# Optimization experiments

Measured on AMD Instinct MI355X. Metric: run time of the kernel, lower is better.

Reference implementation:

```python
import jax, jax.numpy as jnp
import numpy as np

L = 65536   # path length
D = 6       # path channels
K = 4       # signature truncation depth (max of sig_orders)


def setup_inputs() -> dict:
    key = jax.random.key(0)
    # scale keeps high-order signature terms numerically tame over 65k steps
    x = jax.random.normal(key, (L, D), dtype=jnp.float32) * 0.05
    return {"x": x}


def _signature(x):
    """Truncated path signature (levels 1..K), flattened, via Chen's relation.

    Signature of one linear segment with increment dx is exp(dx) in the
    tensor algebra: level k term = dx^{(x)k} / k!.  Full-path signature is the
    Chen (tensor-algebra) product of the per-segment exponentials, computed
    with a left-fold scan over increments.
    """
    dx = x[1:] - x[:-1]                       # (N, D) increments
    N = dx.shape[0]
    # Vectorized exp(dx) levels: E[k-1] = dx^{(x)k}/k!, flattened (N, D^k)
    E = [dx]
    for k in range(2, K + 1):
        Ek = jnp.einsum('na,nb->nab', E[-1], dx).reshape(N, -1) / k
        E.append(Ek)

    S0 = tuple(jnp.zeros((D ** (k + 1),), dtype=x.dtype) for k in range(K))

    def chen(S, e):
        # T_k = S_k + e_k + sum_{i=1}^{k-1} S_i (x) e_{k-i}   (S_0 = e_0 = 1)
        T = []
        for k in range(K):
            t = S[k] + e[k]
            for i in range(k):
                t = t + jnp.einsum('a,b->ab', S[i], e[k - 1 - i]).reshape(-1)
            T.append(t)
        return tuple(T), None

    S, _ = jax.lax.scan(chen, S0, tuple(E))
    # flatten levels 1..K: shape (D + D^2 + ... + D^K,) = (1554,)
    return jnp.concatenate(S)


def reference(x):
    return _signature(x)
```

## Files before the change

### kernel.cpp

```cpp
#include <hip/hip_runtime.h>

#define DIM 6
#define NSEG 65535
#define CH 32
#define NCHUNK 2048

#define PSTRIDE 1568
#define PL1 0
#define PL2 8
#define PL3 48
#define PL4 264

__global__ __launch_bounds__(64) void sig_fold(const float* __restrict__ x,
                                               float* __restrict__ part) {
    __shared__ float dxs[CH * 8];
    const int t = threadIdx.x;
    const int c = blockIdx.x;
    const int j0 = c * CH;
    const int cnt = min(CH, NSEG - j0);

    for (int f = t; f < CH * 8; f += 64) dxs[f] = 0.f;
    __syncthreads();
    const float* xb = x + (size_t)j0 * DIM;
    for (int f = t; f < cnt * DIM; f += 64) {
        int j = f / 6, k = f - j * 6;
        dxs[j * 8 + k] = xb[f + 6] - xb[f];
    }
    __syncthreads();

    const int ab = (t < 36) ? t : 35;
    const int a = ab / 6, b = ab - a * 6;
    const float* dxap = dxs + a;
    const float* dxbp = dxs + b;

    float r4[36], r3[6], r2 = 0.f, s1 = 0.f;
#pragma unroll
    for (int i = 0; i < 36; ++i) r4[i] = 0.f;
#pragma unroll
    for (int i = 0; i < 6; ++i) r3[i] = 0.f;

#pragma unroll 2
    for (int j = 0; j < CH; ++j) {
        const float4 q0 = *(const float4*)(dxs + j * 8);
        const float2 q1 = *(const float2*)(dxs + j * 8 + 4);
        const float dxv[6] = {q0.x, q0.y, q0.z, q0.w, q1.x, q1.y};
        const float dxa = dxap[j * 8];
        const float dxb = dxbp[j * 8];

        float t2 = fmaf(dxb, fmaf(dxa, (1.f / 12.f), s1 * (1.f / 3.f)), r2);
        float t2h = 0.5f * t2;
        float w[6];
#pragma unroll
        for (int cc = 0; cc < 6; ++cc) w[cc] = fmaf(t2h, dxv[cc], r3[cc]);
#pragma unroll
        for (int cc = 0; cc < 6; ++cc)
#pragma unroll
            for (int d = 0; d < 6; ++d)
                r4[cc * 6 + d] = fmaf(w[cc], dxv[d], r4[cc * 6 + d]);
        float t3 = fmaf(dxa, (1.f / 3.f), s1);
        float v = fmaf(0.5f * t3, dxb, r2);
#pragma unroll
        for (int cc = 0; cc < 6; ++cc) r3[cc] = fmaf(v, dxv[cc], r3[cc]);
        r2 = fmaf(fmaf(0.5f, dxa, s1), dxb, r2);
        s1 += dxa;
    }

    if (t < 36) {
        float* P = part + (size_t)c * PSTRIDE;
        if (a == b) P[PL1 + a] = s1;
        P[PL2 + ab] = r2;
        float* p3 = P + PL3 + ab * 6;
        *(float2*)(p3 + 0) = make_float2(r3[0], r3[1]);
        *(float2*)(p3 + 2) = make_float2(r3[2], r3[3]);
        *(float2*)(p3 + 4) = make_float2(r3[4], r3[5]);
        float* p4 = P + PL4 + ab * 36;
#pragma unroll
        for (int i = 0; i < 9; ++i)
            *(float4*)(p4 + 4 * i) =
                make_float4(r4[4 * i], r4[4 * i + 1], r4[4 * i + 2], r4[4 * i + 3]);
    }
}

__global__ __launch_bounds__(64) void sig_comb(const float* __restrict__ in,
                                               float* __restrict__ out,
                                               int R, int flat_out) {
    const int t = threadIdx.x;
    const int ab = (t < 36) ? t : 35;
    const int a = ab / 6, b = ab - a * 6;
    const float* base = in + (size_t)blockIdx.x * R * PSTRIDE;

    float r4[36], r3[6], r2, s1;
    {
        const float* P = base;
        s1 = P[PL1 + a];
        r2 = P[PL2 + ab];
        const float* p3 = P + PL3 + ab * 6;
#pragma unroll
        for (int i = 0; i < 3; ++i) {
            float2 q = *(const float2*)(p3 + 2 * i);
            r3[2 * i] = q.x; r3[2 * i + 1] = q.y;
        }
        const float* p4 = P + PL4 + ab * 36;
#pragma unroll
        for (int i = 0; i < 9; ++i) {
            float4 q = *(const float4*)(p4 + 4 * i);
            r4[4 * i] = q.x; r4[4 * i + 1] = q.y;
            r4[4 * i + 2] = q.z; r4[4 * i + 3] = q.w;
        }
    }

    for (int r = 1; r < R; ++r) {
        const float* U = base + (size_t)r * PSTRIDE;
        float b1[6];
#pragma unroll
        for (int d = 0; d < 6; ++d) b1[d] = U[PL1 + d];
        float b2[36];
#pragma unroll
        for (int i = 0; i < 9; ++i) {
            float4 q = *(const float4*)(U + PL2 + 4 * i);
            b2[4 * i] = q.x; b2[4 * i + 1] = q.y;
            b2[4 * i + 2] = q.z; b2[4 * i + 3] = q.w;
        }
        float b1a = U[PL1 + a];
        float b1b = U[PL1 + b];
        float b2ab = U[PL2 + ab];
        float b2rb[6];
        {
            const float* p = U + PL2 + b * 6;
#pragma unroll
            for (int i = 0; i < 3; ++i) {
                float2 q = *(const float2*)(p + 2 * i);
                b2rb[2 * i] = q.x; b2rb[2 * i + 1] = q.y;
            }
        }
        float b3ab[6];
        {
            const float* p = U + PL3 + ab * 6;
#pragma unroll
            for (int i = 0; i < 3; ++i) {
                float2 q = *(const float2*)(p + 2 * i);
                b3ab[2 * i] = q.x; b3ab[2 * i + 1] = q.y;
            }
        }
        float b3b[36];
        {
            const float* p = U + PL3 + b * 36;
#pragma unroll
            for (int i = 0; i < 9; ++i) {
                float4 q = *(const float4*)(p + 4 * i);
                b3b[4 * i] = q.x; b3b[4 * i + 1] = q.y;
                b3b[4 * i + 2] = q.z; b3b[4 * i + 3] = q.w;
            }
        }
        float b4[36];
        {
            const float* p = U + PL4 + ab * 36;
#pragma unroll
            for (int i = 0; i < 9; ++i) {
                float4 q = *(const float4*)(p + 4 * i);
                b4[4 * i] = q.x; b4[4 * i + 1] = q.y;
                b4[4 * i + 2] = q.z; b4[4 * i + 3] = q.w;
            }
        }

#pragma unroll
        for (int cc = 0; cc < 6; ++cc)
#pragma unroll
            for (int d = 0; d < 6; ++d) {
                const int cd = cc * 6 + d;
                float v = r4[cd] + b4[cd];
                v = fmaf(r3[cc], b1[d], v);
                v = fmaf(r2, b2[cd], v);
                r4[cd] = fmaf(s1, b3b[cd], v);
            }
#pragma unroll
        for (int cc = 0; cc < 6; ++cc) {
            float v = r3[cc] + b3ab[cc];
            v = fmaf(r2, b1[cc], v);
            r3[cc] = fmaf(s1, b2rb[cc], v);
        }
        r2 = fmaf(s1, b1b, r2 + b2ab);
        s1 += b1a;
    }

    if (t < 36) {
        if (flat_out) {
            float* O = out;
            if (a == b) O[a] = s1;
            O[6 + ab] = r2;
            float* o3 = O + 42 + ab * 6;
#pragma unroll
            for (int i = 0; i < 3; ++i)
                *(float2*)(o3 + 2 * i) = make_float2(r3[2 * i], r3[2 * i + 1]);
            float* o4 = O + 258 + ab * 36;
#pragma unroll
            for (int i = 0; i < 18; ++i)
                *(float2*)(o4 + 2 * i) = make_float2(r4[2 * i], r4[2 * i + 1]);
        } else {
            float* P = out + (size_t)blockIdx.x * PSTRIDE;
            if (a == b) P[PL1 + a] = s1;
            P[PL2 + ab] = r2;
            float* p3 = P + PL3 + ab * 6;
#pragma unroll
            for (int i = 0; i < 3; ++i)
                *(float2*)(p3 + 2 * i) = make_float2(r3[2 * i], r3[2 * i + 1]);
            float* p4 = P + PL4 + ab * 36;
#pragma unroll
            for (int i = 0; i < 9; ++i)
                *(float4*)(p4 + 4 * i) =
                    make_float4(r4[4 * i], r4[4 * i + 1], r4[4 * i + 2], r4[4 * i + 3]);
        }
    }
}

extern "C" void kernel_launch(void* const* d_in, const int* in_sizes, int n_in,
                              void* d_out, int out_size, void* d_ws, size_t ws_size,
                              hipStream_t stream) {
    const float* x = (const float*)d_in[0];
    float* out = (float*)d_out;
    float* ws0 = (float*)d_ws;
    float* ws1 = ws0 + (size_t)NCHUNK * PSTRIDE;
    float* ws2 = ws1 + (size_t)256 * PSTRIDE;

    sig_fold<<<NCHUNK, 64, 0, stream>>>(x, ws0);
    sig_comb<<<256, 64, 0, stream>>>(ws0, ws1, 8, 0);
    sig_comb<<<16, 64, 0, stream>>>(ws1, ws2, 16, 0);
    sig_comb<<<1, 64, 0, stream>>>(ws2, out, 16, 1);
}
```

Measured before the change: 114.3 us.

## Stage combine inputs in LDS, use 4-level 8-way tree, select dx via masks

The combine kernel now copies its R partial signatures into shared memory with coalesced float4 loads before the sequential Chen-product loop, so the many per-thread loads hit LDS instead of global memory. The reduction tree changes from 256→16→1 with fan-in 16 to 256→32→4→1 with fan-in 8, which fits the shared buffer and shortens each block's serial chain at the cost of one extra launch. In the fold kernel, per-thread dx[a] and dx[b] are picked from the broadcast row with mask FMAs instead of separate indexed LDS reads, and the loop is unrolled further. The risks are higher LDS use per block, an extra launch, and more VALU work in the fold loop.

```diff
diff --git a/kernel.cpp b/kernel.cpp
--- a/kernel.cpp
+++ b/kernel.cpp
@@ -30,8 +30,12 @@
 
     const int ab = (t < 36) ? t : 35;
     const int a = ab / 6, b = ab - a * 6;
-    const float* dxap = dxs + a;
-    const float* dxbp = dxs + b;
+    float ma[6], mb[6];
+#pragma unroll
+    for (int k = 0; k < 6; ++k) {
+        ma[k] = (a == k) ? 1.f : 0.f;
+        mb[k] = (b == k) ? 1.f : 0.f;
+    }
 
     float r4[36], r3[6], r2 = 0.f, s1 = 0.f;
 #pragma unroll
@@ -39,13 +43,17 @@
 #pragma unroll
     for (int i = 0; i < 6; ++i) r3[i] = 0.f;
 
-#pragma unroll 2
+#pragma unroll 4
     for (int j = 0; j < CH; ++j) {
         const float4 q0 = *(const float4*)(dxs + j * 8);
         const float2 q1 = *(const float2*)(dxs + j * 8 + 4);
         const float dxv[6] = {q0.x, q0.y, q0.z, q0.w, q1.x, q1.y};
-        const float dxa = dxap[j * 8];
-        const float dxb = dxbp[j * 8];
+        float dxa = 0.f, dxb = 0.f;
+#pragma unroll
+        for (int k = 0; k < 6; ++k) {
+            dxa = fmaf(ma[k], dxv[k], dxa);
+            dxb = fmaf(mb[k], dxv[k], dxb);
+        }
 
         float t2 = fmaf(dxb, fmaf(dxa, (1.f / 12.f), s1 * (1.f / 3.f)), r2);
         float t2h = 0.5f * t2;
@@ -84,14 +92,22 @@
 __global__ __launch_bounds__(64) void sig_comb(const float* __restrict__ in,
                                                float* __restrict__ out,
                                                int R, int flat_out) {
+    __shared__ float U[8 * PSTRIDE];
     const int t = threadIdx.x;
     const int ab = (t < 36) ? t : 35;
     const int a = ab / 6, b = ab - a * 6;
-    const float* base = in + (size_t)blockIdx.x * R * PSTRIDE;
+
+    {
+        const float4* g4 = (const float4*)(in + (size_t)blockIdx.x * R * PSTRIDE);
+        float4* s4 = (float4*)U;
+        const int nf4 = R * (PSTRIDE / 4);
+        for (int i = t; i < nf4; i += 64) s4[i] = g4[i];
+    }
+    __syncthreads();
 
     float r4[36], r3[6], r2, s1;
     {
-        const float* P = base;
+        const float* P = U;
         s1 = P[PL1 + a];
         r2 = P[PL2 + ab];
         const float* p3 = P + PL3 + ab * 6;
@@ -110,23 +126,23 @@
     }
 
     for (int r = 1; r < R; ++r) {
-        const float* U = base + (size_t)r * PSTRIDE;
+        const float* Us = U + r * PSTRIDE;
         float b1[6];
 #pragma unroll
-        for (int d = 0; d < 6; ++d) b1[d] = U[PL1 + d];
+        for (int d = 0; d < 6; ++d) b1[d] = Us[PL1 + d];
         float b2[36];
 #pragma unroll
         for (int i = 0; i < 9; ++i) {
-            float4 q = *(const float4*)(U + PL2 + 4 * i);
+            float4 q = *(const float4*)(Us + PL2 + 4 * i);
             b2[4 * i] = q.x; b2[4 * i + 1] = q.y;
             b2[4 * i + 2] = q.z; b2[4 * i + 3] = q.w;
         }
-        float b1a = U[PL1 + a];
-        float b1b = U[PL1 + b];
-        float b2ab = U[PL2 + ab];
+        float b1a = Us[PL1 + a];
+        float b1b = Us[PL1 + b];
+        float b2ab = Us[PL2 + ab];
         float b2rb[6];
         {
-            const float* p = U + PL2 + b * 6;
+            const float* p = Us + PL2 + b * 6;
 #pragma unroll
             for (int i = 0; i < 3; ++i) {
                 float2 q = *(const float2*)(p + 2 * i);
@@ -135,7 +151,7 @@
         }
         float b3ab[6];
         {
-            const float* p = U + PL3 + ab * 6;
+            const float* p = Us + PL3 + ab * 6;
 #pragma unroll
             for (int i = 0; i < 3; ++i) {
                 float2 q = *(const float2*)(p + 2 * i);
@@ -144,7 +160,7 @@
         }
         float b3b[36];
         {
-            const float* p = U + PL3 + b * 36;
+            const float* p = Us + PL3 + b * 36;
 #pragma unroll
             for (int i = 0; i < 9; ++i) {
                 float4 q = *(const float4*)(p + 4 * i);
@@ -154,7 +170,7 @@
         }
         float b4[36];
         {
-            const float* p = U + PL4 + ab * 36;
+            const float* p = Us + PL4 + ab * 36;
 #pragma unroll
             for (int i = 0; i < 9; ++i) {
                 float4 q = *(const float4*)(p + 4 * i);
@@ -221,9 +237,11 @@
     float* ws0 = (float*)d_ws;
     float* ws1 = ws0 + (size_t)NCHUNK * PSTRIDE;
     float* ws2 = ws1 + (size_t)256 * PSTRIDE;
+    float* ws3 = ws2 + (size_t)32 * PSTRIDE;
 
     sig_fold<<<NCHUNK, 64, 0, stream>>>(x, ws0);
     sig_comb<<<256, 64, 0, stream>>>(ws0, ws1, 8, 0);
-    sig_comb<<<16, 64, 0, stream>>>(ws1, ws2, 16, 0);
-    sig_comb<<<1, 64, 0, stream>>>(ws2, out, 16, 1);
+    sig_comb<<<32, 64, 0, stream>>>(ws1, ws2, 8, 0);
+    sig_comb<<<4, 64, 0, stream>>>(ws2, ws3, 8, 0);
+    sig_comb<<<1, 64, 0, stream>>>(ws3, out, 4, 1);
 }
```

After: 127.0 us. 1.11x slower.
